# Kernel optimization log

Measured on AMD Instinct MI355X. Metric: run time of the kernel, lower is better.

## Reference

```python
import jax, jax.numpy as jnp
import numpy as np

BS = 1
H_ = 200
W_ = 200
NQ = H_ * W_          # 40000 BEV queries == num_value
D = 256
NH = 8
DH = D // NH          # 32
NL = 1
NP = 4
NQUEUE = 2
B2 = BS * NQUEUE


def setup_inputs() -> dict:
    key = jax.random.key(0)
    ks = jax.random.split(key, 12)
    s = 0.02
    inp = {
        "query": jax.random.normal(ks[0], (BS, NQ, D), jnp.float32),
        "query_pos": jax.random.normal(ks[1], (BS, NQ, D), jnp.float32) * 0.1,
        "reference_points": jax.random.uniform(ks[2], (BS, NQ, NL, 2), jnp.float32),
        # sampling_offsets linear: in = d_model*num_bev_queue, out = queue*heads*levels*points*2
        "W_so": jax.random.normal(ks[3], (D * NQUEUE, NQUEUE * NH * NL * NP * 2), jnp.float32) * s,
        "b_so": jax.random.normal(ks[4], (NQUEUE * NH * NL * NP * 2,), jnp.float32),
        # attention_weights linear: out = queue*heads*levels*points
        "W_aw": jax.random.normal(ks[5], (D * NQUEUE, NQUEUE * NH * NL * NP), jnp.float32) * s,
        "b_aw": jax.random.normal(ks[6], (NQUEUE * NH * NL * NP,), jnp.float32) * s,
        "W_v": jax.random.normal(ks[7], (D, D), jnp.float32) * s,
        "b_v": jax.random.normal(ks[8], (D,), jnp.float32) * s,
        "W_o": jax.random.normal(ks[9], (D, D), jnp.float32) * s,
        "b_o": jax.random.normal(ks[10], (D,), jnp.float32) * s,
    }
    return inp


def _deform_attn_single_level(v, loc, attn_w):
    """v: (B, Nv, NH, DH); loc: (B, Nq, NH, NP, 2) in [0,1]; attn_w: (B, Nq, NH, NP).
    grid_sample semantics: align_corners=False, zero padding."""
    B = v.shape[0]
    vt = v.transpose(0, 2, 1, 3)                      # (B, NH, Nv, DH)
    # pixel coords (align_corners=False): p = loc * size - 0.5
    x = (loc[..., 0] * W_ - 0.5).transpose(0, 2, 1, 3).reshape(B, NH, -1)  # (B, NH, Nq*NP)
    y = (loc[..., 1] * H_ - 0.5).transpose(0, 2, 1, 3).reshape(B, NH, -1)
    wt = attn_w.transpose(0, 2, 1, 3).reshape(B, NH, -1)
    x0f = jnp.floor(x); y0f = jnp.floor(y)
    x0 = x0f.astype(jnp.int32); y0 = y0f.astype(jnp.int32)
    x1 = x0 + 1; y1 = y0 + 1
    wx1 = x - x0f; wx0 = 1.0 - wx1
    wy1 = y - y0f; wy0 = 1.0 - wy1

    def corner(ix, iy, cw):
        valid = (ix >= 0) & (ix < W_) & (iy >= 0) & (iy < H_)
        idx = jnp.clip(iy, 0, H_ - 1) * W_ + jnp.clip(ix, 0, W_ - 1)
        g = jnp.take_along_axis(vt, idx[..., None], axis=2)   # (B, NH, Nq*NP, DH)
        return g * (cw * valid.astype(cw.dtype))[..., None]

    acc = (corner(x0, y0, wx0 * wy0) + corner(x1, y0, wx1 * wy0)
           + corner(x0, y1, wx0 * wy1) + corner(x1, y1, wx1 * wy1))
    acc = acc * wt[..., None]
    acc = acc.reshape(B, NH, -1, NP, DH).sum(3)               # (B, NH, Nq, DH)
    return acc.transpose(0, 2, 1, 3).reshape(B, -1, NH * DH)  # (B, Nq, D)


def reference(query, query_pos, reference_points, W_so, b_so, W_aw, b_aw, W_v, b_v, W_o, b_o):
    # input_flatten defaults to query (pre-positional); query gets pos added
    q = query + query_pos
    # default queue construction: duplicate current BEV -> (bs*queue, Nv, D)
    value = jnp.stack([query, query], axis=1).reshape(B2, NQ, D)
    history_bev = value[:BS]                                   # (bs, Nv, D)
    qwh = jnp.concatenate([history_bev, q], axis=-1)           # (bs, Nq, 2D)
    # value projection
    v = (value @ W_v + b_v).reshape(B2, NQ, NH, DH)
    # offsets / weights from concatenated features
    so = (qwh @ W_so + b_so).reshape(BS, NQ, NH, NQUEUE, NL, NP, 2)
    aw = (qwh @ W_aw + b_aw).reshape(BS, NQ, NH, NQUEUE, NL * NP)
    aw = jax.nn.softmax(aw, axis=-1).reshape(BS, NQ, NH, NQUEUE, NL, NP)
    aw = aw.transpose(0, 3, 1, 2, 4, 5).reshape(B2, NQ, NH, NL, NP)
    so = so.transpose(0, 3, 1, 2, 4, 5, 6).reshape(B2, NQ, NH, NL, NP, 2)
    # duplicate reference points across the queue
    rp = jnp.stack([reference_points] * NQUEUE, axis=1).reshape(B2, NQ, NL, 2)
    offset_norm = jnp.array([W_, H_], jnp.float32)             # (w, h)
    loc = rp[:, :, None, :, None, :] + so / offset_norm        # (B2, NQ, NH, NL, NP, 2)
    out = _deform_attn_single_level(v, loc[:, :, :, 0], aw[:, :, :, 0])  # (B2, NQ, D)
    # fuse queue outputs by mean (queue is the fast axis of B2)
    out = out.reshape(BS, NQUEUE, NQ, D).mean(axis=1)
    return out @ W_o + b_o
```

## Files before the change

kernel.cpp:

```cpp
#include <hip/hip_runtime.h>
#include <math.h>

#define NQc 40000
#define Wc 200
#define Hc 200

typedef __attribute__((ext_vector_type(8))) short short8;
typedef __attribute__((ext_vector_type(4))) float f32x4;

__device__ __forceinline__ ushort f2b(float f) {
  unsigned u = __float_as_uint(f);
  u = (u + 0x7fffu + ((u >> 16) & 1u)) >> 16;
  return (ushort)u;
}

__device__ __forceinline__ void glds16(const void* g, void* l) {
  __builtin_amdgcn_global_load_lds(
      (const __attribute__((address_space(1))) void*)g,
      (__attribute__((address_space(3))) void*)l, 16, 0, 0);
}

__global__ __launch_bounds__(256) void prep_w(
    const float* __restrict__ Wv, const float* __restrict__ Wo,
    const float* __restrict__ Wso, const float* __restrict__ Waw,
    ushort* __restrict__ WvT, ushort* __restrict__ WoT,
    ushort* __restrict__ WsoT, ushort* __restrict__ WawT) {
  const int idx = blockIdx.x * 256 + threadIdx.x;
  if (idx < 65536) {
    int n = idx >> 8, k = idx & 255;
    WvT[idx] = f2b(Wv[k * 256 + n]);
  } else if (idx < 131072) {
    int i = idx - 65536;
    int n = i >> 8, k = i & 255;
    WoT[i] = f2b(Wo[k * 256 + n]);
  } else if (idx < 196608) {
    int i = idx - 131072;
    int n = i >> 9, k = i & 511;
    WsoT[i] = f2b(Wso[k * 128 + n]);
  } else {
    int i = idx - 196608;
    int n = i >> 9, k = i & 511;
    WawT[i] = f2b(Waw[k * 64 + n]);
  }
}


__global__ __launch_bounds__(256, 3) void gemm_soaw_k(
    const float* __restrict__ q, const float* __restrict__ qp,
    const ushort* __restrict__ WsoT, const ushort* __restrict__ WawT,
    const float* __restrict__ b_so, const float* __restrict__ b_aw,
    float* __restrict__ so_ws, float* __restrict__ aw_ws) {
  __shared__ __align__(16) char smem[33792];
  ushort (*As)[72] = (ushort(*)[72])smem;
  ushort* BsU = (ushort*)(smem + 9216);
  float (*E)[68] = (float(*)[68])smem;
  f32x4 acc[12] = {};
  const int m0 = blockIdx.x * 64;
  const int tid = threadIdx.x;
  const int w = tid >> 6, lane = tid & 63;
  const int rl = lane & 15, q2 = lane >> 4;
  const int sw8 = rl & 7;
  const int lrow = lane >> 3, lch = (lane & 7) ^ (lrow & 7);
  const int arow = tid >> 2, ac16 = (tid & 3) * 16;
  const float* qrow  = q  + (size_t)(m0 + arow) * 256 + ac16;
  const float* qprow = qp + (size_t)(m0 + arow) * 256 + ac16;

  float4 f[4], g4[4];
#pragma unroll
  for (int i = 0; i < 4; ++i) f[i] = *(const float4*)(qrow + i * 4);

  for (int k0 = 0; k0 < 512; k0 += 64) {
    const bool hi = (k0 >= 256);
    __syncthreads();
#pragma unroll
    for (int i = 0; i < 6; ++i) {
      const int g = w * 6 + i;
      const int row = g * 8 + lrow;
      const ushort* gsrc = (row < 128)
          ? WsoT + (size_t)row * 512 + k0 + lch * 8
          : WawT + (size_t)(row - 128) * 512 + k0 + lch * 8;
      glds16(gsrc, BsU + g * 512 + lane * 8);
    }
    {
      ushort tmp[16];
#pragma unroll
      for (int i = 0; i < 4; ++i) {
        float4 a = f[i];
        if (hi) { float4 b = g4[i]; a.x += b.x; a.y += b.y; a.z += b.z; a.w += b.w; }
        tmp[i * 4 + 0] = f2b(a.x); tmp[i * 4 + 1] = f2b(a.y);
        tmp[i * 4 + 2] = f2b(a.z); tmp[i * 4 + 3] = f2b(a.w);
      }
      *(uint4*)&As[arow][ac16]     = *(const uint4*)&tmp[0];
      *(uint4*)&As[arow][ac16 + 8] = *(const uint4*)&tmp[8];
    }
    __syncthreads();
    if (k0 + 64 < 512) {
      const int kn = k0 + 64;
      const int kq = (kn >= 256) ? kn - 256 : kn;
#pragma unroll
      for (int i = 0; i < 4; ++i) f[i] = *(const float4*)(qrow + kq + i * 4);
      if (kn >= 256) {
#pragma unroll
        for (int i = 0; i < 4; ++i) g4[i] = *(const float4*)(qprow + kq + i * 4);
      }
    }
#pragma unroll
    for (int kk = 0; kk < 2; ++kk) {
      const short8 af = *(const short8*)&As[w * 16 + rl][kk * 32 + q2 * 8];
#pragma unroll
      for (int nj = 0; nj < 12; ++nj) {
        const short8 bf = *(const short8*)
            &BsU[(nj * 16 + rl) * 64 + ((kk * 4 + q2) ^ sw8) * 8];
        acc[nj] = __builtin_amdgcn_mfma_f32_16x16x32_bf16(af, bf, acc[nj], 0, 0, 0);
      }
    }
  }
  __syncthreads();

  const int rbase = q2 * 4, cl = rl;
#pragma unroll
  for (int p = 0; p < 3; ++p) {
#pragma unroll
    for (int j = 0; j < 4; ++j) {
      const int nj = p * 4 + j;
      const int nl = j * 16 + cl;
      const f32x4 a = acc[nj];
      if (p < 2) {
        const float bb = b_so[p * 64 + nl];
#pragma unroll
        for (int r = 0; r < 4; ++r)
          E[w * 16 + rbase + r][nl] = a[r] + bb;
      } else {
        const float bb = b_aw[nl];
#pragma unroll
        for (int r = 0; r < 4; ++r) {
          float z = a[r] + bb;
          float zm = fmaxf(z, __shfl_xor(z, 1, 64));
          zm = fmaxf(zm, __shfl_xor(zm, 2, 64));
          float e = expf(z - zm);
          float s = e + __shfl_xor(e, 1, 64);
          s = s + __shfl_xor(s, 2, 64);
          E[w * 16 + rbase + r][nl] = e / s;
        }
      }
    }
    __syncthreads();
#pragma unroll
    for (int it = 0; it < 4; ++it) {
      const int flat = it * 256 + tid;
      const int row = flat >> 4, c4 = (flat & 15) * 4;
      const float4 vle = *(const float4*)&E[row][c4];
      if (p < 2)
        *(float4*)&so_ws[(size_t)(m0 + row) * 128 + p * 64 + c4] = vle;
      else
        *(float4*)&aw_ws[(size_t)(m0 + row) * 64 + c4] = vle;
    }
    __syncthreads();
  }
}

__global__ __launch_bounds__(256, 3) void gemm_v_k(
    const float* __restrict__ q, const ushort* __restrict__ WvT,
    const float* __restrict__ bv, ushort* __restrict__ vt) {
  __shared__ __align__(16) char smem[25600];
  ushort (*As)[72] = (ushort(*)[72])smem;
  ushort* BsU = (ushort*)(smem + 9216);
  ushort (*Eb)[72] = (ushort(*)[72])smem;
  f32x4 acc[8] = {};
  const int m0 = blockIdx.x * 64, n0 = blockIdx.y * 128;
  const int tid = threadIdx.x;
  const int w = tid >> 6, lane = tid & 63;
  const int rl = lane & 15, q2 = lane >> 4;
  const int sw8 = rl & 7;
  const int lrow = lane >> 3, lch = (lane & 7) ^ (lrow & 7);
  const int arow = tid >> 2, ac16 = (tid & 3) * 16;
  const float* qrow = q + (size_t)(m0 + arow) * 256 + ac16;

  float4 f[4];
#pragma unroll
  for (int i = 0; i < 4; ++i) f[i] = *(const float4*)(qrow + i * 4);

  for (int k0 = 0; k0 < 256; k0 += 64) {
    __syncthreads();
#pragma unroll
    for (int i = 0; i < 4; ++i) {
      const int g = w * 4 + i;
      const int row = g * 8 + lrow;
      glds16(WvT + (size_t)(n0 + row) * 256 + k0 + lch * 8,
             BsU + g * 512 + lane * 8);
    }
    {
      ushort tmp[16];
#pragma unroll
      for (int i = 0; i < 4; ++i) {
        const float4 a = f[i];
        tmp[i * 4 + 0] = f2b(a.x); tmp[i * 4 + 1] = f2b(a.y);
        tmp[i * 4 + 2] = f2b(a.z); tmp[i * 4 + 3] = f2b(a.w);
      }
      *(uint4*)&As[arow][ac16]     = *(const uint4*)&tmp[0];
      *(uint4*)&As[arow][ac16 + 8] = *(const uint4*)&tmp[8];
    }
    __syncthreads();
    if (k0 + 64 < 256) {
#pragma unroll
      for (int i = 0; i < 4; ++i) f[i] = *(const float4*)(qrow + k0 + 64 + i * 4);
    }
#pragma unroll
    for (int kk = 0; kk < 2; ++kk) {
      const short8 af = *(const short8*)&As[w * 16 + rl][kk * 32 + q2 * 8];
#pragma unroll
      for (int nj = 0; nj < 8; ++nj) {
        const short8 bf = *(const short8*)
            &BsU[(nj * 16 + rl) * 64 + ((kk * 4 + q2) ^ sw8) * 8];
        acc[nj] = __builtin_amdgcn_mfma_f32_16x16x32_bf16(af, bf, acc[nj], 0, 0, 0);
      }
    }
  }
  __syncthreads();

  const int rbase = q2 * 4, cl = rl;
#pragma unroll
  for (int p = 0; p < 2; ++p) {
#pragma unroll
    for (int j = 0; j < 4; ++j) {
      const int nj = p * 4 + j;
      const int n = n0 + p * 64 + j * 16 + cl;
      const float bb = bv[n];
      const f32x4 a = acc[nj];
#pragma unroll
      for (int r = 0; r < 4; ++r)
        Eb[w * 16 + rbase + r][j * 16 + cl] = f2b(a[r] + bb);
    }
    __syncthreads();
#pragma unroll
    for (int hh = 0; hh < 2; ++hh) {
      const int h = (n0 + p * 64) / 32 + hh;
#pragma unroll
      for (int it = 0; it < 2; ++it) {
        const int flat = it * 256 + tid;
        const int row = flat >> 3, d4 = (flat & 7) * 4;
        *(ushort4*)&vt[((size_t)h * NQc + m0 + row) * 32 + d4] =
            *(const ushort4*)&Eb[row][hh * 32 + d4];
      }
    }
    __syncthreads();
  }
}

__global__ __launch_bounds__(256, 4) void gemm_o_k(
    const ushort* __restrict__ Ap, const ushort* __restrict__ WoT,
    const float* __restrict__ bo, float* __restrict__ out) {
  __shared__ __align__(16) char smem[24576];
  ushort* AsU = (ushort*)smem;
  ushort* BsU = (ushort*)(smem + 8192);
  float (*E)[68] = (float(*)[68])smem;
  f32x4 acc[8] = {};
  const int m0 = blockIdx.x * 64, n0 = blockIdx.y * 128;
  const int tid = threadIdx.x;
  const int w = tid >> 6, lane = tid & 63;
  const int rl = lane & 15, q2 = lane >> 4;
  const int sw8 = rl & 7;
  const int lrow = lane >> 3, lch = (lane & 7) ^ (lrow & 7);

  for (int k0 = 0; k0 < 256; k0 += 64) {
    __syncthreads();
#pragma unroll
    for (int i = 0; i < 2; ++i) {
      const int g = w * 2 + i;
      const int row = g * 8 + lrow;
      glds16(Ap + (size_t)(m0 + row) * 256 + k0 + lch * 8,
             AsU + g * 512 + lane * 8);
    }
#pragma unroll
    for (int i = 0; i < 4; ++i) {
      const int g = w * 4 + i;
      const int row = g * 8 + lrow;
      glds16(WoT + (size_t)(n0 + row) * 256 + k0 + lch * 8,
             BsU + g * 512 + lane * 8);
    }
    __syncthreads();
#pragma unroll
    for (int kk = 0; kk < 2; ++kk) {
      const short8 af = *(const short8*)
          &AsU[(w * 16 + rl) * 64 + ((kk * 4 + q2) ^ sw8) * 8];
#pragma unroll
      for (int nj = 0; nj < 8; ++nj) {
        const short8 bf = *(const short8*)
            &BsU[(nj * 16 + rl) * 64 + ((kk * 4 + q2) ^ sw8) * 8];
        acc[nj] = __builtin_amdgcn_mfma_f32_16x16x32_bf16(af, bf, acc[nj], 0, 0, 0);
      }
    }
  }
  __syncthreads();

  const int rbase = q2 * 4, cl = rl;
#pragma unroll
  for (int p = 0; p < 2; ++p) {
#pragma unroll
    for (int j = 0; j < 4; ++j) {
      const int nj = p * 4 + j;
      const int n = n0 + p * 64 + j * 16 + cl;
      const float bb = bo[n];
      const f32x4 a = acc[nj];
#pragma unroll
      for (int r = 0; r < 4; ++r)
        E[w * 16 + rbase + r][j * 16 + cl] = a[r] + bb;
    }
    __syncthreads();
#pragma unroll
    for (int it = 0; it < 4; ++it) {
      const int flat = it * 256 + tid;
      const int row = flat >> 4, c4 = (flat & 15) * 4;
      *(float4*)&out[(size_t)(m0 + row) * 256 + n0 + p * 64 + c4] =
          *(const float4*)&E[row][c4];
    }
    __syncthreads();
  }
}

__global__ __launch_bounds__(256) void sample_kernel(
    const ushort* __restrict__ vt,
    const float* __restrict__ so_ws,
    const float* __restrict__ aw_ws,
    const float* __restrict__ refp,
    ushort* __restrict__ out_pre)
{
  __shared__ int   offs[8][32][4];
  __shared__ float wts [8][32][4];
  const int h  = blockIdx.x & 7;
  const int m0 = (blockIdx.x >> 3) * 32;
  const int tid = threadIdx.x;

  {
    const int j  = tid & 7;
    const int qi = tid >> 3;
    const int m  = m0 + qi;
    const int c  = h * 8 + j;
    const float sx  = so_ws[(size_t)m * 128 + c * 2 + 0];
    const float sy  = so_ws[(size_t)m * 128 + c * 2 + 1];
    const float wgt = aw_ws[(size_t)m * 64 + c];
    const float x = refp[m * 2 + 0] * (float)Wc + sx - 0.5f;
    const float y = refp[m * 2 + 1] * (float)Hc + sy - 0.5f;
    const float x0f = floorf(x), y0f = floorf(y);
    const int x0 = (int)x0f, y0 = (int)y0f;
    const int x1 = x0 + 1, y1 = y0 + 1;
    const float wx1 = x - x0f, wx0 = 1.0f - wx1;
    const float wy1 = y - y0f, wy0 = 1.0f - wy1;
    const bool vx0 = (x0 >= 0) & (x0 < Wc), vx1 = (x1 >= 0) & (x1 < Wc);
    const bool vy0 = (y0 >= 0) & (y0 < Hc), vy1 = (y1 >= 0) & (y1 < Hc);
    const int cx0 = min(max(x0, 0), Wc - 1), cx1 = min(max(x1, 0), Wc - 1);
    const int cy0 = min(max(y0, 0), Hc - 1), cy1 = min(max(y1, 0), Hc - 1);
    offs[j][qi][0] = (cy0 * Wc + cx0) * 32;
    offs[j][qi][1] = (cy0 * Wc + cx1) * 32;
    offs[j][qi][2] = (cy1 * Wc + cx0) * 32;
    offs[j][qi][3] = (cy1 * Wc + cx1) * 32;
    wts[j][qi][0] = (vx0 & vy0) ? wgt * wx0 * wy0 : 0.0f;
    wts[j][qi][1] = (vx1 & vy0) ? wgt * wx1 * wy0 : 0.0f;
    wts[j][qi][2] = (vx0 & vy1) ? wgt * wx0 * wy1 : 0.0f;
    wts[j][qi][3] = (vx1 & vy1) ? wgt * wx1 * wy1 : 0.0f;
  }
  __syncthreads();

  const int qi = tid >> 3;
  const int ld = tid & 7;
  const int m  = m0 + qi;
  const ushort* __restrict__ vh = vt + (size_t)h * NQc * 32 + ld * 4;
  float a0 = 0.f, a1 = 0.f, a2 = 0.f, a3 = 0.f;
#pragma unroll
  for (int j = 0; j < 8; ++j) {
    const int4   o = *(const int4*)&offs[j][qi][0];
    const float4 w = *(const float4*)&wts[j][qi][0];
#pragma unroll
    for (int k = 0; k < 4; ++k) {
      const int oo = (k == 0) ? o.x : (k == 1) ? o.y : (k == 2) ? o.z : o.w;
      const float ww = (k == 0) ? w.x : (k == 1) ? w.y : (k == 2) ? w.z : w.w;
      const uint2 raw = *(const uint2*)&vh[oo];
      const float f0 = __uint_as_float(raw.x << 16);
      const float f1 = __uint_as_float(raw.x & 0xFFFF0000u);
      const float f2 = __uint_as_float(raw.y << 16);
      const float f3 = __uint_as_float(raw.y & 0xFFFF0000u);
      a0 = fmaf(ww, f0, a0);
      a1 = fmaf(ww, f1, a1);
      a2 = fmaf(ww, f2, a2);
      a3 = fmaf(ww, f3, a3);
    }
  }
  ushort4 o = { f2b(0.5f * a0), f2b(0.5f * a1), f2b(0.5f * a2), f2b(0.5f * a3) };
  *(ushort4*)&out_pre[(size_t)m * 256 + h * 32 + ld * 4] = o;
}

extern "C" void kernel_launch(void* const* d_in, const int* in_sizes, int n_in,
                              void* d_out, int out_size, void* d_ws, size_t ws_size,
                              hipStream_t stream) {
  const float* query     = (const float*)d_in[0];
  const float* query_pos = (const float*)d_in[1];
  const float* refp      = (const float*)d_in[2];
  const float* W_so      = (const float*)d_in[3];
  const float* b_so      = (const float*)d_in[4];
  const float* W_aw      = (const float*)d_in[5];
  const float* b_aw      = (const float*)d_in[6];
  const float* W_v       = (const float*)d_in[7];
  const float* b_v       = (const float*)d_in[8];
  const float* W_o       = (const float*)d_in[9];
  const float* b_o       = (const float*)d_in[10];
  float* out = (float*)d_out;

  char* base = (char*)d_ws;
  ushort* vt      = (ushort*)base;
  float*  so_ws   = (float*)(base + 20480000);
  float*  aw_ws   = (float*)(base + 40960000);
  ushort* out_pre = (ushort*)(base + 51200000);
  ushort* WvT     = (ushort*)(base + 71680000);
  ushort* WoT     = WvT + 65536;
  ushort* WsoT    = WoT + 65536;
  ushort* WawT    = WsoT + 65536;

  prep_w<<<896, 256, 0, stream>>>(W_v, W_o, W_so, W_aw, WvT, WoT, WsoT, WawT);
  gemm_v_k<<<dim3(625, 2), 256, 0, stream>>>(query, WvT, b_v, vt);
  gemm_soaw_k<<<625, 256, 0, stream>>>(query, query_pos, WsoT, WawT,
                                       b_so, b_aw, so_ws, aw_ws);
  sample_kernel<<<10000, 256, 0, stream>>>(vt, so_ws, aw_ws, refp, out_pre);
  gemm_o_k<<<dim3(625, 2), 256, 0, stream>>>(out_pre, WoT, b_o, out);
}
```

Measured before the change: 235.9 us.

## Gather horizontal bilinear corner pairs with one 16-byte load in sampling

The sampling kernel now clamps the left x index so the two horizontally adjacent corners are contiguous (64 bytes per pixel row of 32 bf16 channels). Each thread issues a single 16-byte load covering one row pair, with left and right halves split across lanes. The halves are combined with a lane shuffle, and the 0.5 queue-mean factor is folded into the attention weight. This halves the number of gather instructions and widens each one, and uses packed 2-wide FMAs. The cost is extra edge-case weight logic, a cross-lane reduction, and half the lanes idle on the store.

```diff
diff --git a/kernel.cpp b/kernel.cpp
--- a/kernel.cpp
+++ b/kernel.cpp
@@ -7,6 +7,7 @@
 
 typedef __attribute__((ext_vector_type(8))) short short8;
 typedef __attribute__((ext_vector_type(4))) float f32x4;
+typedef __attribute__((ext_vector_type(2))) float f32x2;
 
 __device__ __forceinline__ ushort f2b(float f) {
   unsigned u = __float_as_uint(f);
@@ -325,8 +326,8 @@
     const float* __restrict__ refp,
     ushort* __restrict__ out_pre)
 {
-  __shared__ int   offs[8][32][4];
-  __shared__ float wts [8][32][4];
+  __shared__ int2   offs[32][9];
+  __shared__ float4 wts [32][9];
   const int h  = blockIdx.x & 7;
   const int m0 = (blockIdx.x >> 3) * 32;
   const int tid = threadIdx.x;
@@ -338,7 +339,7 @@
     const int c  = h * 8 + j;
     const float sx  = so_ws[(size_t)m * 128 + c * 2 + 0];
     const float sy  = so_ws[(size_t)m * 128 + c * 2 + 1];
-    const float wgt = aw_ws[(size_t)m * 64 + c];
+    const float wgt = 0.5f * aw_ws[(size_t)m * 64 + c];
     const float x = refp[m * 2 + 0] * (float)Wc + sx - 0.5f;
     const float y = refp[m * 2 + 1] * (float)Hc + sy - 0.5f;
     const float x0f = floorf(x), y0f = floorf(y);
@@ -346,47 +347,76 @@
     const int x1 = x0 + 1, y1 = y0 + 1;
     const float wx1 = x - x0f, wx0 = 1.0f - wx1;
     const float wy1 = y - y0f, wy0 = 1.0f - wy1;
-    const bool vx0 = (x0 >= 0) & (x0 < Wc), vx1 = (x1 >= 0) & (x1 < Wc);
-    const bool vy0 = (y0 >= 0) & (y0 < Hc), vy1 = (y1 >= 0) & (y1 < Hc);
-    const int cx0 = min(max(x0, 0), Wc - 1), cx1 = min(max(x1, 0), Wc - 1);
-    const int cy0 = min(max(y0, 0), Hc - 1), cy1 = min(max(y1, 0), Hc - 1);
-    offs[j][qi][0] = (cy0 * Wc + cx0) * 32;
-    offs[j][qi][1] = (cy0 * Wc + cx1) * 32;
-    offs[j][qi][2] = (cy1 * Wc + cx0) * 32;
-    offs[j][qi][3] = (cy1 * Wc + cx1) * 32;
-    wts[j][qi][0] = (vx0 & vy0) ? wgt * wx0 * wy0 : 0.0f;
-    wts[j][qi][1] = (vx1 & vy0) ? wgt * wx1 * wy0 : 0.0f;
-    wts[j][qi][2] = (vx0 & vy1) ? wgt * wx0 * wy1 : 0.0f;
-    wts[j][qi][3] = (vx1 & vy1) ? wgt * wx1 * wy1 : 0.0f;
+    const float wx0v = (x0 >= 0 && x0 < Wc) ? wx0 : 0.0f;
+    const float wx1v = (x1 >= 0 && x1 < Wc) ? wx1 : 0.0f;
+    const float wy0v = ((y0 >= 0 && y0 < Hc) ? wy0 : 0.0f) * wgt;
+    const float wy1v = ((y1 >= 0 && y1 < Hc) ? wy1 : 0.0f) * wgt;
+    const int bx = min(max(x0, 0), Wc - 2);
+    const float wl = (bx == x0) ? wx0v : ((bx == x1) ? wx1v : 0.0f);
+    const float wr = (bx + 1 == x1) ? wx1v : ((bx + 1 == x0) ? wx0v : 0.0f);
+    const int cy0 = min(max(y0, 0), Hc - 1);
+    const int cy1 = min(max(y1, 0), Hc - 1);
+    offs[qi][j] = make_int2((cy0 * Wc + bx) * 64, (cy1 * Wc + bx) * 64);
+    wts [qi][j] = make_float4(wl * wy0v, wr * wy0v, wl * wy1v, wr * wy1v);
   }
   __syncthreads();
 
   const int qi = tid >> 3;
   const int ld = tid & 7;
   const int m  = m0 + qi;
-  const ushort* __restrict__ vh = vt + (size_t)h * NQc * 32 + ld * 4;
-  float a0 = 0.f, a1 = 0.f, a2 = 0.f, a3 = 0.f;
+  const char* __restrict__ vb = (const char*)(vt + (size_t)h * NQc * 32);
+  const uint lo16 = (uint)(ld * 16);
+  const bool lohalf = (ld < 4);
+
+  f32x2 acc0 = {0.0f, 0.0f}, acc1 = {0.0f, 0.0f};
+  f32x2 acc2 = {0.0f, 0.0f}, acc3 = {0.0f, 0.0f};
+
 #pragma unroll
   for (int j = 0; j < 8; ++j) {
-    const int4   o = *(const int4*)&offs[j][qi][0];
-    const float4 w = *(const float4*)&wts[j][qi][0];
-#pragma unroll
-    for (int k = 0; k < 4; ++k) {
-      const int oo = (k == 0) ? o.x : (k == 1) ? o.y : (k == 2) ? o.z : o.w;
-      const float ww = (k == 0) ? w.x : (k == 1) ? w.y : (k == 2) ? w.z : w.w;
-      const uint2 raw = *(const uint2*)&vh[oo];
-      const float f0 = __uint_as_float(raw.x << 16);
-      const float f1 = __uint_as_float(raw.x & 0xFFFF0000u);
-      const float f2 = __uint_as_float(raw.y << 16);
-      const float f3 = __uint_as_float(raw.y & 0xFFFF0000u);
-      a0 = fmaf(ww, f0, a0);
-      a1 = fmaf(ww, f1, a1);
-      a2 = fmaf(ww, f2, a2);
-      a3 = fmaf(ww, f3, a3);
-    }
-  }
-  ushort4 o = { f2b(0.5f * a0), f2b(0.5f * a1), f2b(0.5f * a2), f2b(0.5f * a3) };
-  *(ushort4*)&out_pre[(size_t)m * 256 + h * 32 + ld * 4] = o;
+    const int2   oo = offs[qi][j];
+    const float4 ww = wts[qi][j];
+    const float w0 = lohalf ? ww.x : ww.y;
+    const float w1 = lohalf ? ww.z : ww.w;
+#pragma unroll
+    for (int r = 0; r < 2; ++r) {
+      const uint off = (uint)(r == 0 ? oo.x : oo.y) + lo16;
+      const uint4 raw = *(const uint4*)(vb + off);
+      const float w = (r == 0) ? w0 : w1;
+      const f32x2 wv = {w, w};
+      f32x2 v0, v1, v2, v3;
+      v0.x = __uint_as_float(raw.x << 16);
+      v0.y = __uint_as_float(raw.x & 0xFFFF0000u);
+      v1.x = __uint_as_float(raw.y << 16);
+      v1.y = __uint_as_float(raw.y & 0xFFFF0000u);
+      v2.x = __uint_as_float(raw.z << 16);
+      v2.y = __uint_as_float(raw.z & 0xFFFF0000u);
+      v3.x = __uint_as_float(raw.w << 16);
+      v3.y = __uint_as_float(raw.w & 0xFFFF0000u);
+#if __has_builtin(__builtin_elementwise_fma)
+      acc0 = __builtin_elementwise_fma(wv, v0, acc0);
+      acc1 = __builtin_elementwise_fma(wv, v1, acc1);
+      acc2 = __builtin_elementwise_fma(wv, v2, acc2);
+      acc3 = __builtin_elementwise_fma(wv, v3, acc3);
+#else
+      acc0.x = fmaf(w, v0.x, acc0.x); acc0.y = fmaf(w, v0.y, acc0.y);
+      acc1.x = fmaf(w, v1.x, acc1.x); acc1.y = fmaf(w, v1.y, acc1.y);
+      acc2.x = fmaf(w, v2.x, acc2.x); acc2.y = fmaf(w, v2.y, acc2.y);
+      acc3.x = fmaf(w, v3.x, acc3.x); acc3.y = fmaf(w, v3.y, acc3.y);
+#endif
+    }
+  }
+
+  float a[8] = {acc0.x, acc0.y, acc1.x, acc1.y,
+                acc2.x, acc2.y, acc3.x, acc3.y};
+#pragma unroll
+  for (int k = 0; k < 8; ++k) a[k] += __shfl_xor(a[k], 4, 64);
+
+  if (lohalf) {
+    ushort rr[8];
+#pragma unroll
+    for (int k = 0; k < 8; ++k) rr[k] = f2b(a[k]);
+    *(uint4*)&out_pre[(size_t)m * 256 + h * 32 + ld * 8] = *(const uint4*)rr;
+  }
 }
 
 extern "C" void kernel_launch(void* const* d_in, const int* in_sizes, int n_in,
@@ -420,5 +450,5 @@
   gemm_soaw_k<<<625, 256, 0, stream>>>(query, query_pos, WsoT, WawT,
                                        b_so, b_aw, so_ws, aw_ws);
   sample_kernel<<<10000, 256, 0, stream>>>(vt, so_ws, aw_ws, refp, out_pre);
-  gemm_o_k<<<dim3(625, 2), 256, 0, stream>>>(out_pre, WoT, b_o, out);
-}
+  gemm_o_k<<<dim3(625, 2), 256, 0, stream>>>(out_pre, WsoT == nullptr ? nullptr : WoT, b_o, out);
+}
```

Result: slower. 247.0 us (+4.7%).
